# Optimization experiments

Hardware: AMD Instinct MI355X
Metric: run time of the kernel (lower is better)

The kernel has to match this reference:

```python
import jax, jax.numpy as jnp
import numpy as np

B, T, C, R = 4, 2048, 2048, 256


def setup_inputs() -> dict:
    key = jax.random.key(0)
    ks = jax.random.split(key, 12)
    s = 0.02
    return {
        "x": jax.random.normal(ks[0], (B, T, C), dtype=jnp.float32),
        "h_state": jnp.zeros((B, C), dtype=jnp.float32),
        "ln_gamma": jnp.ones((C,), dtype=jnp.float32),
        "ln_beta": jnp.zeros((C,), dtype=jnp.float32),
        "wq_a": jax.random.normal(ks[1], (C, R), dtype=jnp.float32) * s,
        "wq_b": jax.random.normal(ks[2], (R, C), dtype=jnp.float32) * s,
        "wk_a": jax.random.normal(ks[3], (C, R), dtype=jnp.float32) * s,
        "wk_b": jax.random.normal(ks[4], (R, C), dtype=jnp.float32) * s,
        "wv_a": jax.random.normal(ks[5], (C, R), dtype=jnp.float32) * s,
        "wv_b": jax.random.normal(ks[6], (R, C), dtype=jnp.float32) * s,
        "out_w": jax.random.normal(ks[7], (C, C), dtype=jnp.float32) * s,
        "out_b": jnp.zeros((C,), dtype=jnp.float32),
        "time_decay": jnp.full((C,), -0.5, dtype=jnp.float32),
    }


def _layernorm(x, gamma, beta, eps=1e-5):
    mu = jnp.mean(x, axis=-1, keepdims=True)
    var = jnp.var(x, axis=-1, keepdims=True)
    return (x - mu) * jax.lax.rsqrt(var + eps) * gamma + beta


def reference(x, h_state, ln_gamma, ln_beta, wq_a, wq_b, wk_a, wk_b, wv_a, wv_b, out_w, out_b, time_decay):
    b, t, c = x.shape
    xn = _layernorm(x, ln_gamma, ln_beta)
    # token shift: mix current with previous token
    x_shift = jnp.concatenate([jnp.zeros((b, 1, c), xn.dtype), xn[:, :-1, :]], axis=1)
    mix = 0.5 * xn + 0.5 * x_shift
    # low-rank projections: (B,T,C) @ (C,R) @ (R,C)
    q = jnp.einsum('btc,cr,rd->btd', mix, wq_a, wq_b)
    k = jnp.einsum('btc,cr,rd->btd', mix, wk_a, wk_b)
    v = jnp.einsum('btc,cr,rd->btd', mix, wv_a, wv_b)
    decay = jnp.exp(-jnp.exp(time_decay))  # (C,)

    kv = (k * v).transpose(1, 0, 2)          # (T,B,C)
    sq = jax.nn.sigmoid(q).transpose(1, 0, 2)  # (T,B,C)

    def step(h, inp):
        kv_t, sq_t = inp
        h = decay * h + kv_t
        return h, sq_t * h

    h_final, ys = jax.lax.scan(step, h_state, (kv, sq))
    out = ys.transpose(1, 0, 2)               # (B,T,C)
    out = jnp.einsum('btc,dc->btd', out, out_w) + out_b
    return out, h_final
```

## Files before the change

### kernel.cpp

```cpp
#include <hip/hip_runtime.h>


typedef __attribute__((ext_vector_type(8))) __bf16 bf16x8;
typedef __attribute__((ext_vector_type(4))) float f32x4;

static constexpr int Bb = 4, Tt = 2048, Cc = 2048, Rr = 256;
static constexpr int Mrows = Bb * Tt;
static constexpr int NCH = 32, CLEN = 64;

__device__ __forceinline__ unsigned short f2bf(float f) {
  union { float f; unsigned u; } a; a.f = f;
  unsigned r = (a.u + 0x7FFFu + ((a.u >> 16) & 1u)) >> 16;
  return (unsigned short)r;
}
__device__ __forceinline__ float bf2f(unsigned short h) {
  union { unsigned u; float f; } a; a.u = ((unsigned)h) << 16;
  return a.f;
}

__device__ __forceinline__ void gload16(const void* g, void* l) {
  __builtin_amdgcn_global_load_lds(
      (const __attribute__((address_space(1))) void*)g,
      (__attribute__((address_space(3))) void*)l, 16, 0, 0);
}

__global__ void prep_weights(const float* __restrict__ wqa, const float* __restrict__ wka,
                             const float* __restrict__ wva, const float* __restrict__ wqb,
                             const float* __restrict__ wkb, const float* __restrict__ wvb,
                             const float* __restrict__ ow,  const float* __restrict__ td,
                             unsigned short* __restrict__ waT, unsigned short* __restrict__ wbT,
                             unsigned short* __restrict__ owT, float* __restrict__ decay,
                             float* __restrict__ decayL) {
  const int g = blockIdx.x * blockDim.x + threadIdx.x;
  const int stride = gridDim.x * blockDim.x;
  for (int i = g; i < 3 * Rr * Cc; i += stride) {
    int c = i & (Cc - 1); int jj = i >> 11; int p = jj >> 8; int r = jj & (Rr - 1);
    const float* w = (p == 0) ? wqa : ((p == 1) ? wka : wva);
    waT[i] = f2bf(w[(size_t)c * Rr + r]);
  }
  for (int i = g; i < 3 * Cc * Rr; i += stride) {
    int r = i & (Rr - 1); int d = (i >> 8) & (Cc - 1); int p = i >> 19;
    const float* w = (p == 0) ? wqb : ((p == 1) ? wkb : wvb);
    wbT[i] = f2bf(w[(size_t)r * Cc + d]);
  }
  for (int i = g; i < Cc * Cc; i += stride) owT[i] = f2bf(ow[i]);
  for (int i = g; i < Cc; i += stride) {
    float e = expf(td[i]);
    decay[i] = expf(-e);
    decayL[i] = expf(-(float)CLEN * e);
  }
}

__global__ void ln_stats_kernel(const float* __restrict__ x, float* __restrict__ stats) {
  const int row = blockIdx.x;
  const float* xr = x + (size_t)row * Cc;
  float sum = 0.f, sq = 0.f;
  for (int i = threadIdx.x; i < Cc / 4; i += 256) {
    float4 v = ((const float4*)xr)[i];
    sum += v.x + v.y + v.z + v.w;
    sq  += v.x * v.x + v.y * v.y + v.z * v.z + v.w * v.w;
  }
  for (int off = 32; off; off >>= 1) {
    sum += __shfl_down(sum, off);
    sq  += __shfl_down(sq, off);
  }
  __shared__ float s[8];
  if ((threadIdx.x & 63) == 0) { s[(threadIdx.x >> 6) * 2] = sum; s[(threadIdx.x >> 6) * 2 + 1] = sq; }
  __syncthreads();
  if (threadIdx.x == 0) {
    float ts = 0.f, tq = 0.f;
    for (int wv = 0; wv < 4; ++wv) { ts += s[wv * 2]; tq += s[wv * 2 + 1]; }
    float mean = ts * (1.0f / Cc);
    float var  = tq * (1.0f / Cc) - mean * mean;
    stats[row * 2] = mean;
    stats[row * 2 + 1] = rsqrtf(var + 1e-5f);
  }
}

__global__ void mix_kernel(const float* __restrict__ x, const float* __restrict__ stats,
                           const float* __restrict__ gamma, const float* __restrict__ beta,
                           unsigned short* __restrict__ mix) {
  const int total4 = Mrows * (Cc / 4);
  for (int i = blockIdx.x * blockDim.x + threadIdx.x; i < total4; i += gridDim.x * blockDim.x) {
    const int c4 = i & (Cc / 4 - 1);
    const int m  = i >> 9;
    const int t  = m & (Tt - 1);
    const float4 xv = ((const float4*)x)[i];
    const float mu = stats[2 * m], rs = stats[2 * m + 1];
    const float4 g  = ((const float4*)gamma)[c4];
    const float4 bb = ((const float4*)beta)[c4];
    float mx = (xv.x - mu) * rs * g.x + bb.x;
    float my = (xv.y - mu) * rs * g.y + bb.y;
    float mz = (xv.z - mu) * rs * g.z + bb.z;
    float mw = (xv.w - mu) * rs * g.w + bb.w;
    if (t > 0) {
      const float4 pv = ((const float4*)x)[i - Cc / 4];
      const float pmu = stats[2 * (m - 1)], prs = stats[2 * (m - 1) + 1];
      mx = 0.5f * (mx + (pv.x - pmu) * prs * g.x + bb.x);
      my = 0.5f * (my + (pv.y - pmu) * prs * g.y + bb.y);
      mz = 0.5f * (mz + (pv.z - pmu) * prs * g.z + bb.z);
      mw = 0.5f * (mw + (pv.w - pmu) * prs * g.w + bb.w);
    } else {
      mx *= 0.5f; my *= 0.5f; mz *= 0.5f; mw *= 0.5f;
    }
    ushort4 o;
    o.x = f2bf(mx); o.y = f2bf(my); o.z = f2bf(mz); o.w = f2bf(mw);
    ((ushort4*)mix)[i] = o;
  }
}

template <bool STORE_BF16, bool ADD_BIAS>
__global__ __launch_bounds__(256, 2) void gemm_tile(
    const unsigned short* __restrict__ A, int lda,
    const unsigned short* __restrict__ Bt, int ldb,
    void* __restrict__ Cout, int ldc, int K,
    const float* __restrict__ bias) {
  __shared__ unsigned short As[128 * 64];
  __shared__ unsigned short Bs[128 * 64];
  const int tid = threadIdx.x;
  const int lane = tid & 63;
  const int w = tid >> 6;
  const int wr = w >> 1, wc = w & 1;
  const int fr = lane & 15, fq = lane >> 4;
  const long n0 = (long)blockIdx.x * 128;
  const long m0 = (long)blockIdx.y * 128;

  f32x4 acc[4][4];
#pragma unroll
  for (int i = 0; i < 4; ++i)
#pragma unroll
    for (int j = 0; j < 4; ++j) acc[i][j] = (f32x4){0.f, 0.f, 0.f, 0.f};

  const int srow = tid >> 3;
  const int scol = (tid & 7) * 8;
  const unsigned short* Ag = A + (m0 + srow) * (long)lda + scol;
  const unsigned short* Bg = Bt + (n0 + srow) * (long)ldb + scol;

  for (int kt = 0; kt < K; kt += 64) {
#pragma unroll
    for (int r = 0; r < 4; ++r) {
      gload16(Ag + (long)(r * 32) * lda + kt, &As[r * 2048 + tid * 8]);
      gload16(Bg + (long)(r * 32) * ldb + kt, &Bs[r * 2048 + tid * 8]);
    }
    __syncthreads();
#pragma unroll
    for (int kk = 0; kk < 64; kk += 32) {
      bf16x8 af[4], bfr[4];
#pragma unroll
      for (int i = 0; i < 4; ++i) af[i] = *(const bf16x8*)&As[(wr * 64 + i * 16 + fr) * 64 + kk + fq * 8];
#pragma unroll
      for (int j = 0; j < 4; ++j) bfr[j] = *(const bf16x8*)&Bs[(wc * 64 + j * 16 + fr) * 64 + kk + fq * 8];
#pragma unroll
      for (int i = 0; i < 4; ++i)
#pragma unroll
        for (int j = 0; j < 4; ++j)
          acc[i][j] = __builtin_amdgcn_mfma_f32_16x16x32_bf16(af[i], bfr[j], acc[i][j], 0, 0, 0);
    }
    __syncthreads();
  }

#pragma unroll
  for (int j = 0; j < 4; ++j) {
    const long col = n0 + wc * 64 + j * 16 + fr;
    const float bv = ADD_BIAS ? bias[col] : 0.0f;
#pragma unroll
    for (int i = 0; i < 4; ++i) {
      const long row0 = m0 + wr * 64 + i * 16 + fq * 4;
#pragma unroll
      for (int r = 0; r < 4; ++r) {
        float val = acc[i][j][r] + bv;
        if (STORE_BF16)
          ((unsigned short*)Cout)[(row0 + r) * ldc + col] = f2bf(val);
        else
          ((float*)Cout)[(row0 + r) * ldc + col] = val;
      }
    }
  }
}

__global__ void scan_phaseA(const unsigned short* __restrict__ k, const unsigned short* __restrict__ v,
                            const float* __restrict__ decay, float* __restrict__ hend) {
  const int g = blockIdx.x * 256 + threadIdx.x;
  const int c = g & (Cc - 1);
  const int j = (g >> 11) & (NCH - 1);
  const int b = g >> 16;
  const float d = decay[c];
  size_t base = ((size_t)(b * Tt + j * CLEN)) * Cc + c;
  float h = 0.f;
#pragma unroll 8
  for (int s = 0; s < CLEN; ++s) {
    size_t idx = base + (size_t)s * Cc;
    float kv = bf2f(k[idx]) * bf2f(v[idx]);
    h = fmaf(d, h, kv);
  }
  hend[(size_t)(b * NCH + j) * Cc + c] = h;
}

__global__ void scan_combine(const float* __restrict__ hend, const float* __restrict__ h0,
                             const float* __restrict__ decayL, float* __restrict__ Hin,
                             float* __restrict__ hfinal) {
  const int g = blockIdx.x * 256 + threadIdx.x;
  const int c = g & (Cc - 1);
  float H = h0[g];
  const float dl = decayL[c];
  const int b = g >> 11;
  for (int j = 0; j < NCH; ++j) {
    size_t idx = (size_t)(b * NCH + j) * Cc + c;
    Hin[idx] = H;
    H = fmaf(dl, H, hend[idx]);
  }
  hfinal[g] = H;
}

__global__ void scan_phaseB(const unsigned short* __restrict__ q, const unsigned short* __restrict__ k,
                            const unsigned short* __restrict__ v, const float* __restrict__ decay,
                            const float* __restrict__ Hin, unsigned short* __restrict__ ys) {
  const int g = blockIdx.x * 256 + threadIdx.x;
  const int c = g & (Cc - 1);
  const int j = (g >> 11) & (NCH - 1);
  const int b = g >> 16;
  const float d = decay[c];
  float h = Hin[(size_t)(b * NCH + j) * Cc + c];
  size_t base = ((size_t)(b * Tt + j * CLEN)) * Cc + c;
#pragma unroll 4
  for (int s = 0; s < CLEN; ++s) {
    size_t idx = base + (size_t)s * Cc;
    float kv = bf2f(k[idx]) * bf2f(v[idx]);
    h = fmaf(d, h, kv);
    float qq = bf2f(q[idx]);
    float sg = 1.f / (1.f + expf(-qq));
    ys[idx] = f2bf(sg * h);
  }
}

extern "C" void kernel_launch(void* const* d_in, const int* in_sizes, int n_in,
                              void* d_out, int out_size, void* d_ws, size_t ws_size,
                              hipStream_t stream) {
  const float* x   = (const float*)d_in[0];
  const float* h0  = (const float*)d_in[1];
  const float* gam = (const float*)d_in[2];
  const float* bet = (const float*)d_in[3];
  const float* wqa = (const float*)d_in[4];
  const float* wqb = (const float*)d_in[5];
  const float* wka = (const float*)d_in[6];
  const float* wkb = (const float*)d_in[7];
  const float* wva = (const float*)d_in[8];
  const float* wvb = (const float*)d_in[9];
  const float* ow  = (const float*)d_in[10];
  const float* ob  = (const float*)d_in[11];
  const float* td  = (const float*)d_in[12];
  float* out = (float*)d_out;

  char* ws = (char*)d_ws;
  unsigned short* waT   = (unsigned short*)(ws + 0);
  unsigned short* wbT   = (unsigned short*)(ws + 3145728);
  unsigned short* owT   = (unsigned short*)(ws + 6291456);
  float*          decay = (float*)(ws + 14680064);
  float*          decayL= (float*)(ws + 14688256);
  float*          stats = (float*)(ws + 14696448);
  unsigned short* mixb  = (unsigned short*)(ws + 14761984);
  unsigned short* tmp   = (unsigned short*)(ws + 48316416);
  unsigned short* vp    = (unsigned short*)(ws + 60899328);
  float*          hend  = (float*)(ws + 94453760);
  float*          Hin   = (float*)(ws + 95502336);
  unsigned short* qp = (unsigned short*)d_out;
  unsigned short* kp = qp + (size_t)Mrows * Cc;
  float* hfinal = out + (size_t)Mrows * Cc;
  unsigned short* ysb = mixb;

  prep_weights<<<1024, 256, 0, stream>>>(wqa, wka, wva, wqb, wkb, wvb, ow, td,
                                         waT, wbT, owT, decay, decayL);
  ln_stats_kernel<<<Mrows, 256, 0, stream>>>(x, stats);
  mix_kernel<<<2048, 256, 0, stream>>>(x, stats, gam, bet, mixb);

  gemm_tile<true, false><<<dim3(768 / 128, Mrows / 128), 256, 0, stream>>>(
      mixb, Cc, waT, Cc, tmp, 768, Cc, nullptr);
  gemm_tile<true, false><<<dim3(Cc / 128, Mrows / 128), 256, 0, stream>>>(
      tmp + 0, 768, wbT + 0 * Cc * Rr, Rr, qp, Cc, Rr, nullptr);
  gemm_tile<true, false><<<dim3(Cc / 128, Mrows / 128), 256, 0, stream>>>(
      tmp + 256, 768, wbT + 1 * Cc * Rr, Rr, kp, Cc, Rr, nullptr);
  gemm_tile<true, false><<<dim3(Cc / 128, Mrows / 128), 256, 0, stream>>>(
      tmp + 512, 768, wbT + 2 * Cc * Rr, Rr, vp, Cc, Rr, nullptr);

  scan_phaseA<<<(Bb * NCH * Cc) / 256, 256, 0, stream>>>(kp, vp, decay, hend);
  scan_combine<<<(Bb * Cc) / 256, 256, 0, stream>>>(hend, h0, decayL, Hin, hfinal);
  scan_phaseB<<<(Bb * NCH * Cc) / 256, 256, 0, stream>>>(qp, kp, vp, decay, Hin, ysb);

  gemm_tile<false, true><<<dim3(Cc / 128, Mrows / 128), 256, 0, stream>>>(
      ysb, Cc, owT, Cc, out, Cc, Cc, ob);
}
```

Measured before the change: 302.2 us.

## Add 256x256 pipelined GEMM kernel and batch the three rank-up projections

Adds a new 512-thread GEMM with 256x256 tiles, a 4-stage LDS ring fed by global_load_lds, split A/B prefetches interleaved with MFMA halves, and s_setprio around the math. It also uses an XCD-aware block swizzle. The three q/k/v rank-up GEMMs become a single launch indexed by projection, and the output GEMM uses the same kernel. The goal is more reuse per tile, overlap of loads with compute, and fewer launches, at the cost of higher register pressure (128 accumulators per lane) and coarser tiles (256 blocks for the output GEMM).

New measurement: 274.4 us. 9.2% less time.

```diff
diff --git a/kernel.cpp b/kernel.cpp
--- a/kernel.cpp
+++ b/kernel.cpp
@@ -178,6 +178,124 @@
   }
 }
 
+template <bool STORE_BF16, bool ADD_BIAS>
+__global__ __launch_bounds__(512, 2) void gemm_pipe(
+    const unsigned short* __restrict__ A0p, long lda, long aStrideP,
+    const unsigned short* __restrict__ B0p, long ldb, long bStrideP,
+    void* c0, void* c1, void* c2, long ldc, int K,
+    const float* __restrict__ bias, int nbx, int nby) {
+  __shared__ unsigned short lds[4 * 16384];
+  const int tid = threadIdx.x;
+  const int nwg = gridDim.x;
+  const int id = blockIdx.x;
+  const int q = nwg >> 3;
+  const int swz = (id & 7) * q + (id >> 3);
+  const int per = nbx * nby;
+  const int p = swz / per;
+  const int r2 = swz - p * per;
+  const int mblk = r2 / nbx;
+  const int nblk = r2 - mblk * nbx;
+  const unsigned short* A  = A0p + (long)p * aStrideP;
+  const unsigned short* Bt = B0p + (long)p * bStrideP;
+  void* Cout = (p == 0) ? c0 : (p == 1 ? c1 : c2);
+  const long m0 = (long)mblk * 256, n0 = (long)nblk * 256;
+
+  const int lane = tid & 63, wid = tid >> 6;
+  const int wm = wid >> 2, wn = wid & 3;
+  const int fr = lane & 15, fq = lane >> 4;
+
+  const int srow = tid >> 2;
+  const int scolE = (tid & 3) * 8;
+  const unsigned short* Ag = A + (m0 + srow) * lda + scolE;
+  const unsigned short* Bg = Bt + (n0 + srow) * ldb + scolE;
+
+  const unsigned short* aBase = &lds[(wm * 128 + fr) * 32 + fq * 8];
+  const unsigned short* bBase = &lds[8192 + (wn * 64 + fr) * 32 + fq * 8];
+
+  f32x4 acc[8][4];
+#pragma unroll
+  for (int i = 0; i < 8; ++i)
+#pragma unroll
+    for (int j = 0; j < 4; ++j) acc[i][j] = (f32x4){0.f, 0.f, 0.f, 0.f};
+
+  const int NT = K >> 5;
+
+  auto stageA = [&](int t) {
+    unsigned short* d = &lds[(t & 3) * 16384 + tid * 8];
+    const long kt = (long)t * 32;
+    gload16(Ag + kt, d);
+    gload16(Ag + 128 * lda + kt, d + 4096);
+  };
+  auto stageB = [&](int t) {
+    unsigned short* d = &lds[(t & 3) * 16384 + 8192 + tid * 8];
+    const long kt = (long)t * 32;
+    gload16(Bg + kt, d);
+    gload16(Bg + 128 * ldb + kt, d + 4096);
+  };
+
+  stageA(0); stageB(0);
+  stageA(1); stageB(1);
+  stageA(2); stageB(2);
+
+  for (int t = 0; t < NT; ++t) {
+    const int rem = NT - 1 - t;
+    if (rem >= 2)      asm volatile("s_waitcnt vmcnt(8)" ::: "memory");
+    else if (rem == 1) asm volatile("s_waitcnt vmcnt(4)" ::: "memory");
+    else               asm volatile("s_waitcnt vmcnt(0)" ::: "memory");
+    __builtin_amdgcn_s_barrier();
+
+    const unsigned short* ab = aBase + (t & 3) * 16384;
+    const unsigned short* bb = bBase + (t & 3) * 16384;
+
+    bf16x8 bf[4];
+#pragma unroll
+    for (int j = 0; j < 4; ++j) bf[j] = *(const bf16x8*)(bb + j * 512);
+    bf16x8 af[4];
+#pragma unroll
+    for (int i = 0; i < 4; ++i) af[i] = *(const bf16x8*)(ab + i * 512);
+    if (t + 3 < NT) stageA(t + 3);
+    __builtin_amdgcn_s_barrier();
+    __builtin_amdgcn_s_setprio(1);
+#pragma unroll
+    for (int i = 0; i < 4; ++i)
+#pragma unroll
+      for (int j = 0; j < 4; ++j)
+        acc[i][j] = __builtin_amdgcn_mfma_f32_16x16x32_bf16(af[i], bf[j], acc[i][j], 0, 0, 0);
+    __builtin_amdgcn_s_setprio(0);
+    __builtin_amdgcn_s_barrier();
+
+#pragma unroll
+    for (int i = 0; i < 4; ++i) af[i] = *(const bf16x8*)(ab + (4 + i) * 512);
+    if (t + 3 < NT) stageB(t + 3);
+    __builtin_amdgcn_s_barrier();
+    __builtin_amdgcn_s_setprio(1);
+#pragma unroll
+    for (int i = 0; i < 4; ++i)
+#pragma unroll
+      for (int j = 0; j < 4; ++j)
+        acc[4 + i][j] = __builtin_amdgcn_mfma_f32_16x16x32_bf16(af[i], bf[j], acc[4 + i][j], 0, 0, 0);
+    __builtin_amdgcn_s_setprio(0);
+  }
+
+#pragma unroll
+  for (int j = 0; j < 4; ++j) {
+    const long col = n0 + wn * 64 + j * 16 + fr;
+    const float bv = ADD_BIAS ? bias[col] : 0.0f;
+#pragma unroll
+    for (int i = 0; i < 8; ++i) {
+      const long row0 = m0 + wm * 128 + i * 16 + fq * 4;
+#pragma unroll
+      for (int r = 0; r < 4; ++r) {
+        float val = acc[i][j][r] + bv;
+        if (STORE_BF16)
+          ((unsigned short*)Cout)[(row0 + r) * ldc + col] = f2bf(val);
+        else
+          ((float*)Cout)[(row0 + r) * ldc + col] = val;
+      }
+    }
+  }
+}
+
 __global__ void scan_phaseA(const unsigned short* __restrict__ k, const unsigned short* __restrict__ v,
                             const float* __restrict__ decay, float* __restrict__ hend) {
   const int g = blockIdx.x * 256 + threadIdx.x;
@@ -275,17 +393,16 @@
 
   gemm_tile<true, false><<<dim3(768 / 128, Mrows / 128), 256, 0, stream>>>(
       mixb, Cc, waT, Cc, tmp, 768, Cc, nullptr);
-  gemm_tile<true, false><<<dim3(Cc / 128, Mrows / 128), 256, 0, stream>>>(
-      tmp + 0, 768, wbT + 0 * Cc * Rr, Rr, qp, Cc, Rr, nullptr);
-  gemm_tile<true, false><<<dim3(Cc / 128, Mrows / 128), 256, 0, stream>>>(
-      tmp + 256, 768, wbT + 1 * Cc * Rr, Rr, kp, Cc, Rr, nullptr);
-  gemm_tile<true, false><<<dim3(Cc / 128, Mrows / 128), 256, 0, stream>>>(
-      tmp + 512, 768, wbT + 2 * Cc * Rr, Rr, vp, Cc, Rr, nullptr);
+
+  gemm_pipe<true, false><<<8 * 32 * 3, 512, 0, stream>>>(
+      tmp, 768, 256, wbT, Rr, (long)Cc * Rr,
+      qp, kp, vp, Cc, Rr, nullptr, 8, 32);
 
   scan_phaseA<<<(Bb * NCH * Cc) / 256, 256, 0, stream>>>(kp, vp, decay, hend);
   scan_combine<<<(Bb * Cc) / 256, 256, 0, stream>>>(hend, h0, decayL, Hin, hfinal);
   scan_phaseB<<<(Bb * NCH * Cc) / 256, 256, 0, stream>>>(qp, kp, vp, decay, Hin, ysb);
 
-  gemm_tile<false, true><<<dim3(Cc / 128, Mrows / 128), 256, 0, stream>>>(
-      ysb, Cc, owT, Cc, out, Cc, Cc, ob);
-}
+  gemm_pipe<false, true><<<8 * 32, 512, 0, stream>>>(
+      ysb, Cc, 0, owT, Cc, 0,
+      out, out, out, Cc, Cc, ob, 8, 32);
+}
```
